# Optimization experiments

Hardware: AMD Instinct MI355X
Metric: run time of the kernel (lower is better)

## Reference

```python
import jax, jax.numpy as jnp
import numpy as np

HEADS = 16
DIM_HEAD = 64


def setup_inputs() -> dict:
    key = jax.random.key(0)
    k1, k2, k3 = jax.random.split(key, 3)
    b, n, dim = 4, 2048, 1024
    inner = HEADS * DIM_HEAD  # 1024
    x = jax.random.normal(k1, (b, n, dim), dtype=jnp.float32)
    # Dense weights, scaled like Glorot-ish init to keep softmax well-behaved
    w_qkv = jax.random.normal(k2, (dim, 3 * inner), dtype=jnp.float32) * (dim ** -0.5)
    w_out = jax.random.normal(k3, (inner, dim), dtype=jnp.float32) * (inner ** -0.5)
    b_out = jnp.zeros((dim,), dtype=jnp.float32)
    return {"x": x, "w_qkv": w_qkv, "w_out": w_out, "b_out": b_out}


def reference(x, w_qkv, w_out, b_out):
    b, n, dim = x.shape
    scale = DIM_HEAD ** -0.5
    qkv = x @ w_qkv  # [b, n, 3*h*d]
    q, k, v = jnp.split(qkv, 3, axis=-1)
    # 'b n (h d) -> b h n d'
    split_heads = lambda t: t.reshape(b, n, HEADS, DIM_HEAD).transpose(0, 2, 1, 3)
    q, k, v = split_heads(q), split_heads(k), split_heads(v)
    sim = jnp.einsum('bhid,bhjd->bhij', q, k) * scale  # [b, h, n, n]
    attn = jax.nn.softmax(sim, axis=-1)
    out = jnp.einsum('bhij,bhjd->bhid', attn, v)  # [b, h, n, d]
    out = out.transpose(0, 2, 1, 3).reshape(b, n, HEADS * DIM_HEAD)
    return out @ w_out + b_out  # dropout rate 0.0 -> identity
```

## Files before the change

kernel.cpp:

```cpp
#include <hip/hip_runtime.h>
#include <cstdint>

#define HEADS 16
#define DH 64
#define SEQ 2048
#define BATCH 4
#define DIM 1024
#define MTOT (BATCH*SEQ)
#define NQKV (3*DIM)

typedef short bf16x8 __attribute__((ext_vector_type(8)));
typedef float f32x4 __attribute__((ext_vector_type(4)));
typedef float f32x16 __attribute__((ext_vector_type(16)));

__device__ __forceinline__ unsigned short f2bf(float f) {
  union { float fv; unsigned int u; } c; c.fv = f;
  unsigned int u = c.u;
  u += 0x7FFFu + ((u >> 16) & 1u);
  return (unsigned short)(u >> 16);
}

__device__ __forceinline__ unsigned int cvtpk(float lo, float hi) {
  unsigned int r;
  asm("v_cvt_pk_bf16_f32 %0, %1, %2" : "=v"(r) : "v"(lo), "v"(hi));
  return r;
}

__device__ __forceinline__ f32x4 mfma16(bf16x8 a, bf16x8 b, f32x4 c) {
  return __builtin_amdgcn_mfma_f32_16x16x32_bf16(a, b, c, 0, 0, 0);
}
__device__ __forceinline__ f32x16 mfma32(bf16x8 a, bf16x8 b, f32x16 c) {
  return __builtin_amdgcn_mfma_f32_32x32x16_bf16(a, b, c, 0, 0, 0);
}

typedef const __attribute__((address_space(1))) unsigned int* gas_ptr;
typedef __attribute__((address_space(3))) unsigned int* las_ptr;
__device__ __forceinline__ void gl2lds16(const void* g, void* l) {
  __builtin_amdgcn_global_load_lds((gas_ptr)g, (las_ptr)l, 16, 0, 0);
}

#define QSCALE 0.18033688011112042f

__global__ __launch_bounds__(256) void cast_f32_bf16(
    const float* __restrict__ in, unsigned short* __restrict__ out, int n4) {
  int i = blockIdx.x * blockDim.x + threadIdx.x;
  if (i >= n4) return;
  float4 v = reinterpret_cast<const float4*>(in)[i];
  uint2 o;
  o.x = (unsigned int)f2bf(v.x) | ((unsigned int)f2bf(v.y) << 16);
  o.y = (unsigned int)f2bf(v.z) | ((unsigned int)f2bf(v.w) << 16);
  reinterpret_cast<uint2*>(out)[i] = o;
}

__global__ __launch_bounds__(256) void transpose_cast(
    const float* __restrict__ in, unsigned short* __restrict__ out, int R, int C) {
  __shared__ float tile[32][33];
  int c0 = blockIdx.x * 32, r0 = blockIdx.y * 32;
  int tx = threadIdx.x & 31, ty = threadIdx.x >> 5;
  for (int i = 0; i < 32; i += 8)
    tile[ty + i][tx] = in[(size_t)(r0 + ty + i) * C + c0 + tx];
  __syncthreads();
  for (int i = 0; i < 32; i += 8)
    out[(size_t)(c0 + ty + i) * R + r0 + tx] = f2bf(tile[tx][ty + i]);
}

__global__ __launch_bounds__(256) void transpose_v(
    const unsigned short* __restrict__ V, unsigned short* __restrict__ Vt) {
  __shared__ unsigned short tile[64][72];
  int n0 = blockIdx.x * 64;
  size_t base = (size_t)blockIdx.y * SEQ * DH;
  int t = threadIdx.x;
  int r = t >> 2, c = (t & 3) * 8;
  *(uint4*)&tile[r][c]      = *(const uint4*)&V[base + (size_t)(n0 + r) * DH + c];
  *(uint4*)&tile[r][c + 32] = *(const uint4*)&V[base + (size_t)(n0 + r) * DH + c + 32];
  __syncthreads();
#pragma unroll
  for (int p = 0; p < 2; p++) {
    alignas(16) unsigned short tmp[8];
#pragma unroll
    for (int i = 0; i < 8; i++) tmp[i] = tile[c + p * 32 + i][r];
    *(uint4*)&Vt[base + (size_t)r * SEQ + n0 + c + p * 32] = *(uint4*)tmp;
  }
}

#define BM 128
#define BN 128
#define BK 64

__global__ __launch_bounds__(256) void gemm_qkv(
    const unsigned short* __restrict__ A, const unsigned short* __restrict__ Bt,
    unsigned short* __restrict__ Q, unsigned short* __restrict__ K,
    unsigned short* __restrict__ V) {
  __shared__ unsigned short sA[BM * BK];
  __shared__ unsigned short sB[BN * BK];
  const int KD = 1024;
  int gid = blockIdx.x + 24 * blockIdx.y;
  int swz = (gid & 7) * 192 + (gid >> 3);
  int m0 = (swz / 24) * BM;
  int n0 = (swz % 24) * BN;
  int t = threadIdx.x;
  int lane = t & 63, w = t >> 6;
  int wm = (w >> 1) * 64, wn = (w & 1) * 64;
  int fr = lane & 15, fg = lane >> 4;

  int srow = w * 8 + (lane >> 3);
  int scol = ((lane & 7) ^ (lane >> 3)) * 8;
  const unsigned short* gA = &A[(size_t)(m0 + srow) * KD + scol];
  const unsigned short* gB = &Bt[(size_t)(n0 + srow) * KD + scol];
  char* lA = (char*)sA + w * 1024;
  char* lB = (char*)sB + w * 1024;

  f32x4 acc[4][4];
#pragma unroll
  for (int i = 0; i < 4; i++)
#pragma unroll
    for (int j = 0; j < 4; j++) { f32x4 z = {0.f, 0.f, 0.f, 0.f}; acc[i][j] = z; }

  for (int k0 = 0; k0 < KD; k0 += BK) {
#pragma unroll
    for (int i = 0; i < 4; i++) {
      gl2lds16(gA + (size_t)i * 32 * KD + k0, lA + i * 4096);
      gl2lds16(gB + (size_t)i * 32 * KD + k0, lB + i * 4096);
    }
    __syncthreads();
#pragma unroll
    for (int ks = 0; ks < 2; ks++) {
      bf16x8 af[4], bfr[4];
#pragma unroll
      for (int mt = 0; mt < 4; mt++)
        af[mt] = *reinterpret_cast<const bf16x8*>(
            &sA[(wm + mt * 16 + fr) * BK + (((ks * 4 + fg) ^ (fr & 7)) * 8)]);
#pragma unroll
      for (int nt = 0; nt < 4; nt++)
        bfr[nt] = *reinterpret_cast<const bf16x8*>(
            &sB[(wn + nt * 16 + fr) * BK + (((ks * 4 + fg) ^ (fr & 7)) * 8)]);
#pragma unroll
      for (int mt = 0; mt < 4; mt++)
#pragma unroll
        for (int nt = 0; nt < 4; nt++)
          acc[mt][nt] = mfma16(af[mt], bfr[nt], acc[mt][nt]);
    }
    __syncthreads();
  }

  int rowq = (lane >> 4) * 4;
  int b = m0 >> 11;
  int nrow0 = (m0 & 2047) + wm + rowq;
#pragma unroll
  for (int nt = 0; nt < 4; nt++) {
    int ncb = n0 + wn + nt * 16;
    int which = ncb >> 10;
    int hdb = ncb & 1023;
    int hh = hdb >> 6;
    int dcol = (hdb & 63) + fr;
    unsigned short* dst = (which == 0) ? Q : (which == 1 ? K : V);
    size_t cbase = ((size_t)(b * HEADS + hh) * SEQ) * DH + dcol;
#pragma unroll
    for (int mt = 0; mt < 4; mt++) {
      f32x4 av = acc[mt][nt];
      if (which == 0) {
        av[0] *= QSCALE; av[1] *= QSCALE; av[2] *= QSCALE; av[3] *= QSCALE;
      }
      size_t idx = cbase + (size_t)(nrow0 + mt * 16) * DH;
      unsigned int u0 = cvtpk(av[0], av[1]);
      unsigned int u1 = cvtpk(av[2], av[3]);
      dst[idx]          = (unsigned short)u0;
      dst[idx + DH]     = (unsigned short)(u0 >> 16);
      dst[idx + 2 * DH] = (unsigned short)u1;
      dst[idx + 3 * DH] = (unsigned short)(u1 >> 16);
    }
  }
}

__global__ __launch_bounds__(256) void gemm_out(
    const unsigned short* __restrict__ A, const unsigned short* __restrict__ Bt,
    const float* __restrict__ bias, float* __restrict__ C) {
  __shared__ unsigned short sA[BM * BK];
  __shared__ unsigned short sB[BN * BK];
  const int KD = 1024;
  int gid = blockIdx.x + 8 * blockIdx.y;
  int swz = (gid & 7) * 64 + (gid >> 3);
  int m0 = (swz / 8) * BM;
  int n0 = (swz % 8) * BN;
  int t = threadIdx.x;
  int lane = t & 63, w = t >> 6;
  int wm = (w >> 1) * 64, wn = (w & 1) * 64;
  int fr = lane & 15, fg = lane >> 4;

  int srow = w * 8 + (lane >> 3);
  int scol = ((lane & 7) ^ (lane >> 3)) * 8;
  const unsigned short* gA = &A[(size_t)(m0 + srow) * KD + scol];
  const unsigned short* gB = &Bt[(size_t)(n0 + srow) * KD + scol];
  char* lA = (char*)sA + w * 1024;
  char* lB = (char*)sB + w * 1024;

  f32x4 acc[4][4];
#pragma unroll
  for (int i = 0; i < 4; i++)
#pragma unroll
    for (int j = 0; j < 4; j++) { f32x4 z = {0.f, 0.f, 0.f, 0.f}; acc[i][j] = z; }

  for (int k0 = 0; k0 < KD; k0 += BK) {
#pragma unroll
    for (int i = 0; i < 4; i++) {
      gl2lds16(gA + (size_t)i * 32 * KD + k0, lA + i * 4096);
      gl2lds16(gB + (size_t)i * 32 * KD + k0, lB + i * 4096);
    }
    __syncthreads();
#pragma unroll
    for (int ks = 0; ks < 2; ks++) {
      bf16x8 af[4], bfr[4];
#pragma unroll
      for (int mt = 0; mt < 4; mt++)
        af[mt] = *reinterpret_cast<const bf16x8*>(
            &sA[(wm + mt * 16 + fr) * BK + (((ks * 4 + fg) ^ (fr & 7)) * 8)]);
#pragma unroll
      for (int nt = 0; nt < 4; nt++)
        bfr[nt] = *reinterpret_cast<const bf16x8*>(
            &sB[(wn + nt * 16 + fr) * BK + (((ks * 4 + fg) ^ (fr & 7)) * 8)]);
#pragma unroll
      for (int mt = 0; mt < 4; mt++)
#pragma unroll
        for (int nt = 0; nt < 4; nt++)
          acc[mt][nt] = mfma16(af[mt], bfr[nt], acc[mt][nt]);
    }
    __syncthreads();
  }

  int rowq = (lane >> 4) * 4;
#pragma unroll
  for (int nt = 0; nt < 4; nt++) {
    int ncol = n0 + wn + nt * 16 + fr;
    float bb = bias[ncol];
    size_t cb = (size_t)(m0 + wm + rowq) * DIM + ncol;
#pragma unroll
    for (int mt = 0; mt < 4; mt++)
#pragma unroll
      for (int r = 0; r < 4; r++)
        C[cb + (size_t)(mt * 16 + r) * DIM] = acc[mt][nt][r] + bb;
  }
}

#define LDA 68

__global__ __launch_bounds__(256, 4) void attention(
    const unsigned short* __restrict__ Qg, const unsigned short* __restrict__ Kg,
    const unsigned short* __restrict__ Vtg, unsigned short* __restrict__ Og) {
  __shared__ unsigned short smem[2 * 64 * 72];
  unsigned short* sK  = smem;
  unsigned short* sVt = smem + 64 * LDA;

  int gid = blockIdx.x + 16 * (blockIdx.y + 16 * blockIdx.z);
  int qb   = (gid >> 3) & 15;
  int pair = ((gid & 7) << 3) | (gid >> 7);
  int h = pair & 15, b = pair >> 4;

  size_t base = (size_t)(b * HEADS + h) * SEQ * DH;
  const unsigned short* Q = Qg + base;
  const unsigned short* K = Kg + base;
  const unsigned short* Vt = Vtg + base;
  int t = threadIdx.x, lane = t & 63, w = t >> 6;
  int m = lane & 31, kh = lane >> 5;
  int q0 = qb * 128 + w * 32;

  bf16x8 qf[4];
#pragma unroll
  for (int kt = 0; kt < 4; kt++)
    qf[kt] = *reinterpret_cast<const bf16x8*>(
        &Q[(size_t)(q0 + m) * DH + kt * 16 + kh * 8]);

  f32x16 oaccT[2];
#pragma unroll
  for (int dh = 0; dh < 2; dh++)
#pragma unroll
    for (int i = 0; i < 16; i++) oaccT[dh][i] = 0.f;
  float rs = 0.f;

  int sr = t >> 2, sc = (t & 3) * 8;

  for (int j0 = 0; j0 < SEQ; j0 += 64) {
    {
      uint4 a0 = *(const uint4*)&K[(size_t)(j0 + sr) * DH + sc];
      uint4 a1 = *(const uint4*)&K[(size_t)(j0 + sr) * DH + sc + 32];
      uint4 b0 = *(const uint4*)&Vt[(size_t)sr * SEQ + j0 + sc];
      uint4 b1 = *(const uint4*)&Vt[(size_t)sr * SEQ + j0 + sc + 32];
      unsigned short* pk0 = &sK[sr * LDA + sc];
      unsigned short* pk1 = &sK[sr * LDA + sc + 32];
      unsigned short* pv0 = &sVt[sr * LDA + sc];
      unsigned short* pv1 = &sVt[sr * LDA + sc + 32];
      *(uint2*)pk0       = make_uint2(a0.x, a0.y);
      *(uint2*)(pk0 + 4) = make_uint2(a0.z, a0.w);
      *(uint2*)pk1       = make_uint2(a1.x, a1.y);
      *(uint2*)(pk1 + 4) = make_uint2(a1.z, a1.w);
      *(uint2*)pv0       = make_uint2(b0.x, b0.y);
      *(uint2*)(pv0 + 4) = make_uint2(b0.z, b0.w);
      *(uint2*)pv1       = make_uint2(b1.x, b1.y);
      *(uint2*)(pv1 + 4) = make_uint2(b1.z, b1.w);
    }
    __syncthreads();

    unsigned int pp[8][2];
#pragma unroll
    for (int jt = 0; jt < 2; jt++) {
      bf16x8 kf[4];
#pragma unroll
      for (int kt = 0; kt < 4; kt++) {
        union { uint2 u[2]; bf16x8 v; } kc;
        const unsigned short* p = &sK[(jt * 32 + m) * LDA + (2 * kt + kh) * 8];
        kc.u[0] = *(const uint2*)p;
        kc.u[1] = *(const uint2*)(p + 4);
        kf[kt] = kc.v;
      }
      f32x16 s;
#pragma unroll
      for (int i = 0; i < 16; i++) s[i] = 0.f;
#pragma unroll
      for (int kt = 0; kt < 4; kt++)
        s = mfma32(kf[kt], qf[kt], s);
      float e[16];
#pragma unroll
      for (int i = 0; i < 16; i++) e[i] = __builtin_amdgcn_exp2f(s[i]);
      float t0 = (e[0] + e[1]) + (e[2] + e[3]);
      float t1 = (e[4] + e[5]) + (e[6] + e[7]);
      float t2 = (e[8] + e[9]) + (e[10] + e[11]);
      float t3 = (e[12] + e[13]) + (e[14] + e[15]);
      rs += (t0 + t1) + (t2 + t3);
#pragma unroll
      for (int sl = 0; sl < 4; sl++) {
        pp[4 * jt + sl][0] = cvtpk(e[4 * sl + 0], e[4 * sl + 1]);
        pp[4 * jt + sl][1] = cvtpk(e[4 * sl + 2], e[4 * sl + 3]);
      }
    }

#pragma unroll
    for (int kb = 0; kb < 4; kb++) {
#pragma unroll
      for (int dh = 0; dh < 2; dh++) {
        union { uint2 u[2]; bf16x8 v; } ac;
        const unsigned short* p = &sVt[(32 * dh + m) * LDA + 16 * kb + 4 * kh];
        ac.u[0] = *(const uint2*)p;
        ac.u[1] = *(const uint2*)(p + 8);
        union { unsigned int u[4]; bf16x8 v; } bc;
        bc.u[0] = pp[2 * kb][0];
        bc.u[1] = pp[2 * kb][1];
        bc.u[2] = pp[2 * kb + 1][0];
        bc.u[3] = pp[2 * kb + 1][1];
        oaccT[dh] = mfma32(ac.v, bc.v, oaccT[dh]);
      }
    }
    __syncthreads();
  }

  float inv;
  {
    float tot = rs + __shfl_xor(rs, 32);
    inv = 1.0f / tot;
  }

  unsigned int* ew = (unsigned int*)smem + (size_t)w * 32 * 36;
#pragma unroll
  for (int dh = 0; dh < 2; dh++)
#pragma unroll
    for (int sl = 0; sl < 4; sl++) {
      unsigned int u0 = cvtpk(oaccT[dh][4 * sl + 0] * inv, oaccT[dh][4 * sl + 1] * inv);
      unsigned int u1 = cvtpk(oaccT[dh][4 * sl + 2] * inv, oaccT[dh][4 * sl + 3] * inv);
      uint2 pk; pk.x = u0; pk.y = u1;
      *(uint2*)&ew[m * 36 + 16 * dh + 4 * sl + 2 * kh] = pk;
    }
  {
    int mr = lane >> 3, ch = lane & 7;
#pragma unroll
    for (int it = 0; it < 4; it++) {
      uint4 vv = *(const uint4*)&ew[(8 * it + mr) * 36 + ch * 4];
      int n = q0 + 8 * it + mr;
      *(uint4*)&Og[((size_t)(b * SEQ + n)) * DIM + h * DH + ch * 8] = vv;
    }
  }
}

extern "C" void kernel_launch(void* const* d_in, const int* in_sizes, int n_in,
                              void* d_out, int out_size, void* d_ws, size_t ws_size,
                              hipStream_t stream) {
  const float* x     = (const float*)d_in[0];
  const float* w_qkv = (const float*)d_in[1];
  const float* w_out = (const float*)d_in[2];
  const float* b_out = (const float*)d_in[3];
  float* out = (float*)d_out;

  char* ws = (char*)d_ws;
  unsigned short* xb     = (unsigned short*)ws; ws += (size_t)MTOT * DIM * 2;
  unsigned short* wqkv_t = (unsigned short*)ws; ws += (size_t)NQKV * DIM * 2;
  unsigned short* wout_t = (unsigned short*)ws; ws += (size_t)DIM * DIM * 2;
  unsigned short* qb_    = (unsigned short*)ws; ws += (size_t)BATCH * HEADS * SEQ * DH * 2;
  unsigned short* kb_    = (unsigned short*)ws; ws += (size_t)BATCH * HEADS * SEQ * DH * 2;
  unsigned short* vb_    = (unsigned short*)ws; ws += (size_t)BATCH * HEADS * SEQ * DH * 2;
  unsigned short* attnb  = (unsigned short*)ws; ws += (size_t)MTOT * DIM * 2;
  unsigned short* vt_    = xb;

  cast_f32_bf16<<<(MTOT * DIM / 4 + 255) / 256, 256, 0, stream>>>(x, xb, MTOT * DIM / 4);
  transpose_cast<<<dim3(NQKV / 32, DIM / 32), 256, 0, stream>>>(w_qkv, wqkv_t, DIM, NQKV);
  transpose_cast<<<dim3(DIM / 32, DIM / 32), 256, 0, stream>>>(w_out, wout_t, DIM, DIM);

  gemm_qkv<<<dim3(NQKV / BN, MTOT / BM), 256, 0, stream>>>(xb, wqkv_t, qb_, kb_, vb_);

  transpose_v<<<dim3(SEQ / 64, BATCH * HEADS), 256, 0, stream>>>(vb_, vt_);

  attention<<<dim3(SEQ / 128, HEADS, BATCH), 256, 0, stream>>>(qb_, kb_, vt_, attnb);

  gemm_out<<<dim3(DIM / BN, MTOT / BM), 256, 0, stream>>>(attnb, wout_t, b_out, out);
}
```

Baseline: 265.0 us.

## Pipeline GEMMs with 4-stage async LDS ring and 256x128 tiles

Both projection GEMMs get a 4-deep ring of LDS buffers with BK=32 stages loaded via global-to-LDS copies. Three stages are in flight at once, and a vmcnt wait plus a barrier replaces the two __syncthreads per iteration. Blocks grow to 512 threads covering 256x128 tiles, with a new XOR swizzle and s_setprio around the MFMA burst. The aim is to hide global load latency and cut barrier overhead, at the cost of more LDS per block (96KB) and lower occupancy.

```diff
diff --git a/kernel.cpp b/kernel.cpp
--- a/kernel.cpp
+++ b/kernel.cpp
@@ -83,72 +83,88 @@
   }
 }
 
-#define BM 128
-#define BN 128
-#define BK 64
-
-__global__ __launch_bounds__(256) void gemm_qkv(
+
+#define STAGE(TT) { \
+    char* _b = (char*)smem + ((TT) & 3) * 24576 + w * 1024; \
+    gl2lds16(gA0 + (size_t)(TT) * 32, _b); \
+    gl2lds16(gA1 + (size_t)(TT) * 32, _b + 8192); \
+    gl2lds16(gB0 + (size_t)(TT) * 32, _b + 16384); }
+
+#define WAITB(N) { \
+    asm volatile("s_waitcnt vmcnt(" #N ")" ::: "memory"); \
+    __builtin_amdgcn_s_barrier(); \
+    __builtin_amdgcn_sched_barrier(0); }
+
+#define GCOMPUTE(T) { \
+    const unsigned short* sAt = smem + ((T) & 3) * 12288; \
+    const unsigned short* sBt = sAt + 8192; \
+    bf16x8 af[4], bv[4]; \
+    _Pragma("unroll") \
+    for (int mt = 0; mt < 4; mt++) \
+      af[mt] = *reinterpret_cast<const bf16x8*>( \
+          &sAt[(wr64 + mt * 16 + fr) * 32 + fchunk]); \
+    _Pragma("unroll") \
+    for (int nt = 0; nt < 4; nt++) \
+      bv[nt] = *reinterpret_cast<const bf16x8*>( \
+          &sBt[(wc64 + nt * 16 + fr) * 32 + fchunk]); \
+    __builtin_amdgcn_s_setprio(1); \
+    _Pragma("unroll") \
+    for (int mt = 0; mt < 4; mt++) \
+      _Pragma("unroll") \
+      for (int nt = 0; nt < 4; nt++) \
+        acc[mt][nt] = mfma16(af[mt], bv[nt], acc[mt][nt]); \
+    __builtin_amdgcn_s_setprio(0); }
+
+#define GEMM_SETUP(Abase, Bbase) \
+  const int KD = 1024; \
+  int t = threadIdx.x; \
+  int lane = t & 63, w = t >> 6; \
+  int wr64 = (w >> 1) * 64;            \
+  int wc64 = (w & 1) * 64;             \
+  int fr = lane & 15, fg = lane >> 4; \
+  int fchunk = (fg ^ ((fr >> 1) & 3)) * 8;    \
+  int lr = lane >> 2; \
+  int cg = ((lane & 3) ^ ((lane >> 3) & 3)) * 8;   \
+  const unsigned short* gA0 = (Abase) + (size_t)(m0 + w * 16 + lr) * KD + cg; \
+  const unsigned short* gA1 = gA0 + (size_t)128 * KD; \
+  const unsigned short* gB0 = (Bbase) + (size_t)(n0 + w * 16 + lr) * KD + cg; \
+  f32x4 acc[4][4]; \
+  _Pragma("unroll") \
+  for (int i = 0; i < 4; i++) \
+    _Pragma("unroll") \
+    for (int j = 0; j < 4; j++) { f32x4 z = {0.f, 0.f, 0.f, 0.f}; acc[i][j] = z; }
+
+#define GEMM_MAINLOOP \
+  STAGE(0); STAGE(1); STAGE(2); \
+  for (int kt = 0; kt < 30; ++kt) { \
+    WAITB(6); \
+    if (kt < 29) STAGE(kt + 3); \
+    GCOMPUTE(kt); \
+  } \
+  WAITB(3); \
+  GCOMPUTE(30); \
+  WAITB(0); \
+  GCOMPUTE(31);
+
+__global__ __launch_bounds__(512, 2) void gemm_qkv(
     const unsigned short* __restrict__ A, const unsigned short* __restrict__ Bt,
     unsigned short* __restrict__ Q, unsigned short* __restrict__ K,
     unsigned short* __restrict__ V) {
-  __shared__ unsigned short sA[BM * BK];
-  __shared__ unsigned short sB[BN * BK];
-  const int KD = 1024;
+  __shared__ unsigned short smem[4 * 12288];
   int gid = blockIdx.x + 24 * blockIdx.y;
-  int swz = (gid & 7) * 192 + (gid >> 3);
-  int m0 = (swz / 24) * BM;
-  int n0 = (swz % 24) * BN;
-  int t = threadIdx.x;
-  int lane = t & 63, w = t >> 6;
-  int wm = (w >> 1) * 64, wn = (w & 1) * 64;
-  int fr = lane & 15, fg = lane >> 4;
-
-  int srow = w * 8 + (lane >> 3);
-  int scol = ((lane & 7) ^ (lane >> 3)) * 8;
-  const unsigned short* gA = &A[(size_t)(m0 + srow) * KD + scol];
-  const unsigned short* gB = &Bt[(size_t)(n0 + srow) * KD + scol];
-  char* lA = (char*)sA + w * 1024;
-  char* lB = (char*)sB + w * 1024;
-
-  f32x4 acc[4][4];
-#pragma unroll
-  for (int i = 0; i < 4; i++)
-#pragma unroll
-    for (int j = 0; j < 4; j++) { f32x4 z = {0.f, 0.f, 0.f, 0.f}; acc[i][j] = z; }
-
-  for (int k0 = 0; k0 < KD; k0 += BK) {
-#pragma unroll
-    for (int i = 0; i < 4; i++) {
-      gl2lds16(gA + (size_t)i * 32 * KD + k0, lA + i * 4096);
-      gl2lds16(gB + (size_t)i * 32 * KD + k0, lB + i * 4096);
-    }
-    __syncthreads();
-#pragma unroll
-    for (int ks = 0; ks < 2; ks++) {
-      bf16x8 af[4], bfr[4];
-#pragma unroll
-      for (int mt = 0; mt < 4; mt++)
-        af[mt] = *reinterpret_cast<const bf16x8*>(
-            &sA[(wm + mt * 16 + fr) * BK + (((ks * 4 + fg) ^ (fr & 7)) * 8)]);
-#pragma unroll
-      for (int nt = 0; nt < 4; nt++)
-        bfr[nt] = *reinterpret_cast<const bf16x8*>(
-            &sB[(wn + nt * 16 + fr) * BK + (((ks * 4 + fg) ^ (fr & 7)) * 8)]);
-#pragma unroll
-      for (int mt = 0; mt < 4; mt++)
-#pragma unroll
-        for (int nt = 0; nt < 4; nt++)
-          acc[mt][nt] = mfma16(af[mt], bfr[nt], acc[mt][nt]);
-    }
-    __syncthreads();
-  }
-
-  int rowq = (lane >> 4) * 4;
+  int swz = (gid & 7) * 96 + (gid >> 3);
+  int m0 = (swz / 24) * 256;
+  int n0 = (swz % 24) * 128;
+
+  GEMM_SETUP(A, Bt)
+  GEMM_MAINLOOP
+
+  int rowq = fg * 4;
   int b = m0 >> 11;
-  int nrow0 = (m0 & 2047) + wm + rowq;
+  int nrow0 = (m0 & 2047) + wr64 + rowq;
 #pragma unroll
   for (int nt = 0; nt < 4; nt++) {
-    int ncb = n0 + wn + nt * 16;
+    int ncb = n0 + wc64 + nt * 16;
     int which = ncb >> 10;
     int hdb = ncb & 1023;
     int hh = hdb >> 6;
@@ -172,67 +188,24 @@
   }
 }
 
-__global__ __launch_bounds__(256) void gemm_out(
+__global__ __launch_bounds__(512, 2) void gemm_out(
     const unsigned short* __restrict__ A, const unsigned short* __restrict__ Bt,
     const float* __restrict__ bias, float* __restrict__ C) {
-  __shared__ unsigned short sA[BM * BK];
-  __shared__ unsigned short sB[BN * BK];
-  const int KD = 1024;
+  __shared__ unsigned short smem[4 * 12288];
   int gid = blockIdx.x + 8 * blockIdx.y;
-  int swz = (gid & 7) * 64 + (gid >> 3);
-  int m0 = (swz / 8) * BM;
-  int n0 = (swz % 8) * BN;
-  int t = threadIdx.x;
-  int lane = t & 63, w = t >> 6;
-  int wm = (w >> 1) * 64, wn = (w & 1) * 64;
-  int fr = lane & 15, fg = lane >> 4;
-
-  int srow = w * 8 + (lane >> 3);
-  int scol = ((lane & 7) ^ (lane >> 3)) * 8;
-  const unsigned short* gA = &A[(size_t)(m0 + srow) * KD + scol];
-  const unsigned short* gB = &Bt[(size_t)(n0 + srow) * KD + scol];
-  char* lA = (char*)sA + w * 1024;
-  char* lB = (char*)sB + w * 1024;
-
-  f32x4 acc[4][4];
-#pragma unroll
-  for (int i = 0; i < 4; i++)
-#pragma unroll
-    for (int j = 0; j < 4; j++) { f32x4 z = {0.f, 0.f, 0.f, 0.f}; acc[i][j] = z; }
-
-  for (int k0 = 0; k0 < KD; k0 += BK) {
-#pragma unroll
-    for (int i = 0; i < 4; i++) {
-      gl2lds16(gA + (size_t)i * 32 * KD + k0, lA + i * 4096);
-      gl2lds16(gB + (size_t)i * 32 * KD + k0, lB + i * 4096);
-    }
-    __syncthreads();
-#pragma unroll
-    for (int ks = 0; ks < 2; ks++) {
-      bf16x8 af[4], bfr[4];
-#pragma unroll
-      for (int mt = 0; mt < 4; mt++)
-        af[mt] = *reinterpret_cast<const bf16x8*>(
-            &sA[(wm + mt * 16 + fr) * BK + (((ks * 4 + fg) ^ (fr & 7)) * 8)]);
-#pragma unroll
-      for (int nt = 0; nt < 4; nt++)
-        bfr[nt] = *reinterpret_cast<const bf16x8*>(
-            &sB[(wn + nt * 16 + fr) * BK + (((ks * 4 + fg) ^ (fr & 7)) * 8)]);
-#pragma unroll
-      for (int mt = 0; mt < 4; mt++)
-#pragma unroll
-        for (int nt = 0; nt < 4; nt++)
-          acc[mt][nt] = mfma16(af[mt], bfr[nt], acc[mt][nt]);
-    }
-    __syncthreads();
-  }
-
-  int rowq = (lane >> 4) * 4;
+  int swz = (gid & 7) * 32 + (gid >> 3);
+  int m0 = (swz / 8) * 256;
+  int n0 = (swz % 8) * 128;
+
+  GEMM_SETUP(A, Bt)
+  GEMM_MAINLOOP
+
+  int rowq = fg * 4;
 #pragma unroll
   for (int nt = 0; nt < 4; nt++) {
-    int ncol = n0 + wn + nt * 16 + fr;
+    int ncol = n0 + wc64 + nt * 16 + fr;
     float bb = bias[ncol];
-    size_t cb = (size_t)(m0 + wm + rowq) * DIM + ncol;
+    size_t cb = (size_t)(m0 + wr64 + rowq) * DIM + ncol;
 #pragma unroll
     for (int mt = 0; mt < 4; mt++)
 #pragma unroll
@@ -401,11 +374,11 @@
   transpose_cast<<<dim3(NQKV / 32, DIM / 32), 256, 0, stream>>>(w_qkv, wqkv_t, DIM, NQKV);
   transpose_cast<<<dim3(DIM / 32, DIM / 32), 256, 0, stream>>>(w_out, wout_t, DIM, DIM);
 
-  gemm_qkv<<<dim3(NQKV / BN, MTOT / BM), 256, 0, stream>>>(xb, wqkv_t, qb_, kb_, vb_);
+  gemm_qkv<<<dim3(24, 32), 512, 0, stream>>>(xb, wqkv_t, qb_, kb_, vb_);
 
   transpose_v<<<dim3(SEQ / 64, BATCH * HEADS), 256, 0, stream>>>(vb_, vt_);
 
   attention<<<dim3(SEQ / 128, HEADS, BATCH), 256, 0, stream>>>(qb_, kb_, vt_, attnb);
 
-  gemm_out<<<dim3(DIM / BN, MTOT / BM), 256, 0, stream>>>(attnb, wout_t, b_out, out);
-}
+  gemm_out<<<dim3(8, 32), 512, 0, stream>>>(attnb, wout_t, b_out, out);
+}
```

Measured after the change: 270.7 us. +2.1%, slower.
